# Kernel optimization log

Measured on AMD Instinct MI355X. Metric: run time of the kernel, lower is better.

The kernel has to match this reference:

```python
import jax, jax.numpy as jnp
import numpy as np

B, K, T, H, D = 16, 49, 256, 512, 512


def setup_inputs() -> dict:
    key = jax.random.key(0)
    ks = jax.random.split(key, 8)
    s = 1.0 / np.sqrt(H)
    return {
        "V": jax.random.normal(ks[0], (B, K, H), jnp.float32),
        "h_t": jax.random.normal(ks[1], (B, T, H), jnp.float32),
        "s_t": jax.random.normal(ks[2], (B, T, H), jnp.float32),
        "Wv": jax.random.normal(ks[3], (H, D), jnp.float32) * s,
        "bv": jnp.zeros((D,), jnp.float32),
        "Wg": jax.random.normal(ks[4], (H, D), jnp.float32) * s,
        "bg": jnp.zeros((D,), jnp.float32),
        "Ws": jax.random.normal(ks[5], (H, D), jnp.float32) * s,
        "bs": jnp.zeros((D,), jnp.float32),
        "Wh": jax.random.normal(ks[6], (D, 1), jnp.float32) * (1.0 / np.sqrt(D)),
        "bh": jnp.zeros((1,), jnp.float32),
    }


def reference(V, h_t, s_t, Wv, bv, Wg, bg, Ws, bs, Wh, bh):
    # projections (dropout is identity in eval)
    cv = V @ Wv + bv                        # [B, K, D]
    cg = h_t @ Wg + bg                      # [B, T, D]
    # content_v: [B, T, K, D] via broadcast add
    content_v = cv[:, None, :, :] + cg[:, :, None, :]
    z_t = (jnp.tanh(content_v) @ Wh + bh)[..., 0]   # [B, T, K]
    alpha_t = jax.nn.softmax(z_t, axis=-1)          # [B, T, K]
    c_t = jnp.einsum('btk,bkh->bth', alpha_t, V)    # [B, T, H]
    # sentinel branch
    content_s = (s_t @ Ws + bs) + cg                # [B, T, D]
    z_ext = jnp.tanh(content_s) @ Wh + bh           # [B, T, 1]
    extended = jnp.concatenate([z_t, z_ext], axis=-1)  # [B, T, K+1]
    alpha_hat = jax.nn.softmax(extended, axis=-1)
    beta_t = alpha_hat[:, :, -1:]                   # [B, T, 1]
    c_hat_t = beta_t * s_t + (1.0 - beta_t) * c_t   # [B, T, H]
    return (c_hat_t, alpha_t, beta_t)
```

## Files before the change

kernel.cpp:

```cpp
#include <hip/hip_runtime.h>
#include <hip/hip_fp16.h>
#include <cstdint>
#include <cstddef>

#define B_ 16
#define K_ 49
#define T_ 256
#define H_ 512
#define D_ 512

#define TANH_SCALE 2.8853900817779268f
#define LOG2E 1.4426950408889634f

typedef _Float16 half8 __attribute__((ext_vector_type(8)));
typedef float floatx4 __attribute__((ext_vector_type(4)));

#define ROWS_A 9088
#define OFF_V 0
#define OFF_H 896
#define OFF_S 4992

__device__ __forceinline__ void async16(const _Float16* g, const _Float16* l) {
    __builtin_amdgcn_global_load_lds(
        (const __attribute__((address_space(1))) unsigned int*)g,
        (__attribute__((address_space(3))) unsigned int*)l, 16, 0, 0);
}

__global__ __launch_bounds__(256) void conv_all(const float* __restrict__ V,
                                                const float* __restrict__ h_t,
                                                const float* __restrict__ s_t,
                                                const float* __restrict__ Wv,
                                                const float* __restrict__ Wg,
                                                const float* __restrict__ Ws,
                                                _Float16* __restrict__ Af16,
                                                _Float16* __restrict__ Wt) {
    __shared__ float tile[32][33];
    int tid = threadIdx.x;
    if (blockIdx.x < 2272) {
        int idx = (blockIdx.x * 256 + tid) * 8;
        int row = idx >> 9;
        int col = idx & 511;
        const float* src;
        if (row < 784)        src = V   + (size_t)row * 512 + col;
        else if (row < 896)   src = nullptr;
        else if (row < 4992)  src = h_t + (size_t)(row - 896) * 512 + col;
        else                  src = s_t + (size_t)(row - 4992) * 512 + col;
        half8 h;
        if (src) {
            float4 f0 = *(const float4*)(src);
            float4 f1 = *(const float4*)(src + 4);
            h[0] = (_Float16)f0.x; h[1] = (_Float16)f0.y;
            h[2] = (_Float16)f0.z; h[3] = (_Float16)f0.w;
            h[4] = (_Float16)f1.x; h[5] = (_Float16)f1.y;
            h[6] = (_Float16)f1.z; h[7] = (_Float16)f1.w;
        } else {
            h = (half8)((_Float16)0.0f);
        }
        *(half8*)(Af16 + idx) = h;
    } else {
        int bid = blockIdx.x - 2272;
        int p = bid >> 8;
        int rem = bid & 255;
        int bx = rem & 15, by = rem >> 4;
        const float* W = (p == 0) ? Wv : (p == 1) ? Wg : Ws;
        _Float16* outp = Wt + (size_t)p * 512 * 512;
        int tx = tid & 31, ty = tid >> 5;
        int c = bx * 32 + tx;
        int rbase = by * 32;
#pragma unroll
        for (int i = 0; i < 4; i++)
            tile[ty + i * 8][tx] = W[(size_t)(rbase + ty + i * 8) * 512 + c];
        __syncthreads();
        int k = rbase + tx;
#pragma unroll
        for (int i = 0; i < 4; i++) {
            int n = bx * 32 + ty + i * 8;
            outp[(size_t)n * 512 + k] = (_Float16)(tile[tx][ty + i * 8] * TANH_SCALE);
        }
    }
}

__global__ __launch_bounds__(256) void gemm_f16(
    const _Float16* __restrict__ Af16, const _Float16* __restrict__ Wt,
    const float* __restrict__ bv, const float* __restrict__ bg2,
    const float* __restrict__ bs, float* __restrict__ cv,
    float* __restrict__ cg, float* __restrict__ cs) {
    __shared__ __align__(16) _Float16 As[2][64 * 64];
    __shared__ __align__(16) _Float16 Bs[2][64 * 64];

    int bid = blockIdx.x;
    int id = (bid & 7) * 142 + (bid >> 3);

    int rowbase; const _Float16* Bt; const float* bias; float* C;
    if (id < 112)       { rowbase = OFF_V;            Bt = Wt;          bias = bv;  C = cv; }
    else if (id < 624)  { id -= 112; rowbase = OFF_H; Bt = Wt + 262144; bias = bg2; C = cg; }
    else                { id -= 624; rowbase = OFF_S; Bt = Wt + 524288; bias = bs;  C = cs; }
    int tm = id >> 3, tn = id & 7;

    int tid = threadIdx.x;
    int wave = tid >> 6, lane = tid & 63;

    const _Float16* gA[2]; int ldsOff[2];
    const _Float16* gB[2];
#pragma unroll
    for (int i = 0; i < 2; i++) {
        int p = i * 256 + tid;
        int ks = p >> 8, x = (p >> 6) & 3, q = (p >> 4) & 3, f = p & 15;
        gA[i] = Af16 + (size_t)(rowbase + tm * 64 + x * 16 + f) * 512 + ks * 32 + q * 8;
        gB[i] = Bt   + (size_t)(tn * 64 + x * 16 + f) * 512 + ks * 32 + q * 8;
        ldsOff[i] = p * 8;
    }

    floatx4 acc[4];
#pragma unroll
    for (int x = 0; x < 4; x++) acc[x] = (floatx4)0.0f;

#pragma unroll
    for (int i = 0; i < 2; i++) async16(gA[i], &As[0][ldsOff[i]]);
#pragma unroll
    for (int i = 0; i < 2; i++) async16(gB[i], &Bs[0][ldsOff[i]]);
    __syncthreads();

    for (int kk = 0; kk < 8; kk++) {
        int cur = kk & 1;
        if (kk < 7) {
#pragma unroll
            for (int i = 0; i < 2; i++) async16(gA[i] + (kk + 1) * 64, &As[cur ^ 1][ldsOff[i]]);
#pragma unroll
            for (int i = 0; i < 2; i++) async16(gB[i] + (kk + 1) * 64, &Bs[cur ^ 1][ldsOff[i]]);
        }

#pragma unroll
        for (int ks = 0; ks < 2; ks++) {
            half8 a[4];
#pragma unroll
            for (int x = 0; x < 4; x++)
                a[x] = *(const half8*)&As[cur][(ks * 256 + x * 64 + lane) * 8];
            half8 b = *(const half8*)&Bs[cur][(ks * 256 + wave * 64 + lane) * 8];
#pragma unroll
            for (int x = 0; x < 4; x++)
                acc[x] = __builtin_amdgcn_mfma_f32_16x16x32_f16(a[x], b, acc[x], 0, 0, 0);
        }

        if (kk < 7) __syncthreads();
    }

    int dn = lane & 15, dq = lane >> 4;
    int colg = tn * 64 + wave * 16 + dn;
    float bc = bias[colg] * TANH_SCALE;
#pragma unroll
    for (int x = 0; x < 4; x++) {
        int rowg = tm * 64 + x * 16 + dq * 4;
#pragma unroll
        for (int r = 0; r < 4; r++)
            C[(size_t)(rowg + r) * 512 + colg] = __builtin_amdgcn_exp2f(acc[x][r] + bc);
    }
}

__device__ __forceinline__ float wave_sum(float v) {
#pragma unroll
    for (int o = 32; o > 0; o >>= 1) v += __shfl_xor(v, o);
    return v;
}
__device__ __forceinline__ float wave_max(float v) {
#pragma unroll
    for (int o = 32; o > 0; o >>= 1) v = fmaxf(v, __shfl_xor(v, o));
    return v;
}

__device__ __forceinline__ float xsum4(float a0, float a1, float a2, float a3, int lane) {
    bool hi = (lane & 32) != 0;
    float t0 = hi ? a0 : a2;
    float t1 = hi ? a1 : a3;
    t0 = __shfl_xor(t0, 32);
    t1 = __shfl_xor(t1, 32);
    if (hi) { a0 = t0; a1 = t1; } else { a2 = t0; a3 = t1; }
    bool h2 = (lane & 16) != 0;
    float u0 = h2 ? a0 : a1;
    float u1 = h2 ? a2 : a3;
    u0 = __shfl_xor(u0, 16);
    u1 = __shfl_xor(u1, 16);
    if (h2) { a0 = u0; a2 = u1; } else { a1 = u0; a3 = u1; }
    float s = (a0 + a1) + (a2 + a3);
#pragma unroll
    for (int o = 8; o > 0; o >>= 1) s += __shfl_xor(s, o);
    return s;
}

#define TB 4
__global__ __launch_bounds__(256) void z_kernel(
    const float* __restrict__ ecv, const float* __restrict__ ecg,
    const float* __restrict__ ecs, const float* __restrict__ V,
    const float* __restrict__ s_t, const float* __restrict__ Wh,
    const float* __restrict__ bh, float* __restrict__ out) {
    int bx = blockIdx.x;
    int b  = bx >> 6;
    int t0 = (bx & 63) << 2;
    int bt0 = b * 256 + t0;
    int tid = threadIdx.x;
    int wave = tid >> 6, lane = tid & 63;

    __shared__ float zl[TB][64];
    __shared__ float4 al4[52];
    __shared__ float bl[TB];

    float whv[8], egv[TB][8];
#pragma unroll
    for (int j = 0; j < 8; j++) whv[j] = Wh[j * 64 + lane];
#pragma unroll
    for (int tt = 0; tt < TB; tt++) {
        const float* cgp = ecg + (size_t)(bt0 + tt) * 512;
#pragma unroll
        for (int j = 0; j < 8; j++) egv[tt][j] = cgp[j * 64 + lane];
    }
    float s8 = 0.0f;
#pragma unroll
    for (int j = 0; j < 8; j++) s8 += whv[j];
    float zbase = wave_sum(s8) + bh[0];

    float rv[8], rn[8];
    {
        const float* rp = ecv + (size_t)(b * 49 + wave) * 512;
#pragma unroll
        for (int j = 0; j < 8; j++) rv[j] = rp[j * 64 + lane];
    }
    for (int task = wave; task < 49; task += 4) {
        int nt = task + 4;
        if (nt < 49) {
            const float* rp = ecv + (size_t)(b * 49 + nt) * 512;
#pragma unroll
            for (int j = 0; j < 8; j++) rn[j] = rp[j * 64 + lane];
        }
        float acc[TB] = {0.0f, 0.0f, 0.0f, 0.0f};
#pragma unroll
        for (int tt = 0; tt < TB; tt++) {
#pragma unroll
            for (int j = 0; j < 8; j++) {
                float t = fmaf(rv[j], egv[tt][j], 1.0f);
                float r = __builtin_amdgcn_rcpf(t);
                acc[tt] = fmaf(whv[j], r, acc[tt]);
            }
        }
        float z = xsum4(acc[0], acc[1], acc[2], acc[3], lane);
        if ((lane & 15) == 0) zl[lane >> 4][task] = zbase - 2.0f * z;
#pragma unroll
        for (int j = 0; j < 8; j++) rv[j] = rn[j];
    }
#pragma unroll
    for (int tt = 0; tt < TB; tt++) {
        if (wave == tt) {
            const float* rp = ecs + (size_t)(bt0 + tt) * 512;
            float acc = 0.0f;
#pragma unroll
            for (int j = 0; j < 8; j++) {
                float t = fmaf(rp[j * 64 + lane], egv[tt][j], 1.0f);
                float r = __builtin_amdgcn_rcpf(t);
                acc = fmaf(whv[j], r, acc);
            }
            float s = wave_sum(acc);
            if (lane == 0) zl[tt][49] = zbase - 2.0f * s;
        }
    }
    __syncthreads();

    {
        int w = wave;
        float z = (lane < 49) ? zl[w][lane] : -3.0e38f;
        float m = wave_max(z);
        float e = (lane < 49) ? __builtin_amdgcn_exp2f((z - m) * LOG2E) : 0.0f;
        float s = wave_sum(e);
        float zext = zl[w][49];
        float m2 = fmaxf(m, zext);
        float sc   = __builtin_amdgcn_exp2f((m - m2) * LOG2E);
        float eext = __builtin_amdgcn_exp2f((zext - m2) * LOG2E);
        float s2 = s * sc + eext;
        float beta = eext / s2;
        if (lane < 49) {
            float a = e / s;
            ((float*)&al4[lane])[w] = a;
            out[(size_t)B_ * T_ * H_ + (size_t)(bt0 + w) * 49 + lane] = a;
        }
        if (lane == 0) {
            bl[w] = beta;
            out[(size_t)B_ * T_ * H_ + (size_t)B_ * T_ * K_ + (bt0 + w)] = beta;
        }
    }
    __syncthreads();

    const float* Vb = V + (size_t)b * 49 * 512;
    float2 accA[TB];
#pragma unroll
    for (int tt = 0; tt < TB; tt++) accA[tt] = make_float2(0.0f, 0.0f);
#pragma unroll 7
    for (int k = 0; k < 49; k++) {
        float4 a4 = al4[k];
        float2 v = *(const float2*)(Vb + (size_t)k * 512 + tid * 2);
        accA[0].x = fmaf(a4.x, v.x, accA[0].x);  accA[0].y = fmaf(a4.x, v.y, accA[0].y);
        accA[1].x = fmaf(a4.y, v.x, accA[1].x);  accA[1].y = fmaf(a4.y, v.y, accA[1].y);
        accA[2].x = fmaf(a4.z, v.x, accA[2].x);  accA[2].y = fmaf(a4.z, v.y, accA[2].y);
        accA[3].x = fmaf(a4.w, v.x, accA[3].x);  accA[3].y = fmaf(a4.w, v.y, accA[3].y);
    }
#pragma unroll
    for (int tt = 0; tt < TB; tt++) {
        float beta = bl[tt];
        float2 sp = *(const float2*)(s_t + (size_t)(bt0 + tt) * 512 + tid * 2);
        float2 o;
        o.x = beta * sp.x + (1.0f - beta) * accA[tt].x;
        o.y = beta * sp.y + (1.0f - beta) * accA[tt].y;
        *(float2*)(out + (size_t)(bt0 + tt) * 512 + tid * 2) = o;
    }
}

extern "C" void kernel_launch(void* const* d_in, const int* in_sizes, int n_in,
                              void* d_out, int out_size, void* d_ws, size_t ws_size,
                              hipStream_t stream) {
    const float* V   = (const float*)d_in[0];
    const float* h_t = (const float*)d_in[1];
    const float* s_t = (const float*)d_in[2];
    const float* Wv  = (const float*)d_in[3];
    const float* bv  = (const float*)d_in[4];
    const float* Wg  = (const float*)d_in[5];
    const float* bg  = (const float*)d_in[6];
    const float* Ws  = (const float*)d_in[7];
    const float* bs  = (const float*)d_in[8];
    const float* Wh  = (const float*)d_in[9];
    const float* bh  = (const float*)d_in[10];
    float* out = (float*)d_out;

    char* ws = (char*)d_ws;
    _Float16* Af16 = (_Float16*)(ws);
    _Float16* Wt   = (_Float16*)(ws + 9306112);
    float* ecv = (float*)(ws + 10878976);
    float* ecg = (float*)(ws + 12713984);
    float* ecs = (float*)(ws + 21102592);

    conv_all<<<3040, 256, 0, stream>>>(V, h_t, s_t, Wv, Wg, Ws, Af16, Wt);
    gemm_f16<<<1136, 256, 0, stream>>>(Af16, Wt, bv, bg, bs, ecv, ecg, ecs);
    z_kernel<<<1024, 256, 0, stream>>>(ecv, ecg, ecs, V, s_t, Wh, bh, out);
}
```

Baseline: 135.7 us.

## Pre-tile fp16 operands into MFMA fragment layout and single-barrier pipeline

The conversion kernel now writes activations and transposed weights in a blocked layout that matches the LDS fragment order, so each GEMM tile stage becomes one contiguous 8KB chunk read with fully coalesced async loads. The GEMM main loop is restructured to use a single explicit vmcnt wait plus barrier per stage, with sched_barriers, and is fully unrolled. This removes strided global reads and one barrier per iteration. The cost is a more complex index computation in the pre-pass, which now does scattered fp16 weight stores.

```diff
diff --git a/kernel.cpp b/kernel.cpp
--- a/kernel.cpp
+++ b/kernel.cpp
@@ -56,14 +56,16 @@
         } else {
             h = (half8)((_Float16)0.0f);
         }
-        *(half8*)(Af16 + idx) = h;
+        int t  = row >> 7, x8 = (row >> 4) & 7, f = row & 15;
+        int kk = col >> 5, q  = (col >> 3) & 3;
+        size_t off = (size_t)t * 65536 + (size_t)kk * 4096 + (size_t)(x8 * 64 + q * 16 + f) * 8;
+        *(half8*)(Af16 + off) = h;
     } else {
         int bid = blockIdx.x - 2272;
         int p = bid >> 8;
         int rem = bid & 255;
         int bx = rem & 15, by = rem >> 4;
         const float* W = (p == 0) ? Wv : (p == 1) ? Wg : Ws;
-        _Float16* outp = Wt + (size_t)p * 512 * 512;
         int tx = tid & 31, ty = tid >> 5;
         int c = bx * 32 + tx;
         int rbase = by * 32;
@@ -72,10 +74,14 @@
             tile[ty + i * 8][tx] = W[(size_t)(rbase + ty + i * 8) * 512 + c];
         __syncthreads();
         int k = rbase + tx;
+        int kk = k >> 5, q = (k >> 3) & 3, e = k & 7;
 #pragma unroll
         for (int i = 0; i < 4; i++) {
             int n = bx * 32 + ty + i * 8;
-            outp[(size_t)n * 512 + k] = (_Float16)(tile[tx][ty + i * 8] * TANH_SCALE);
+            int nt = n >> 7, x8 = (n >> 4) & 7, f = n & 15;
+            size_t off = (size_t)p * 262144 + (size_t)nt * 65536 + (size_t)kk * 4096
+                       + (size_t)(x8 * 64 + q * 16 + f) * 8 + e;
+            Wt[off] = (_Float16)(tile[tx][ty + i * 8] * TANH_SCALE);
         }
     }
 }
@@ -85,8 +91,8 @@
     const float* __restrict__ bv, const float* __restrict__ bg2,
     const float* __restrict__ bs, float* __restrict__ cv,
     float* __restrict__ cg, float* __restrict__ cs) {
-    __shared__ __align__(16) _Float16 As[2][64 * 64];
-    __shared__ __align__(16) _Float16 Bs[2][64 * 64];
+    __shared__ __align__(16) _Float16 As[2][4096];
+    __shared__ __align__(16) _Float16 Bs[2][4096];
 
     int bid = blockIdx.x;
     int id = (bid & 7) * 142 + (bid >> 3);
@@ -100,15 +106,16 @@
     int tid = threadIdx.x;
     int wave = tid >> 6, lane = tid & 63;
 
-    const _Float16* gA[2]; int ldsOff[2];
-    const _Float16* gB[2];
+    int r0 = rowbase + tm * 64;
+    const _Float16* aBase = Af16 + (size_t)(r0 >> 7) * 65536 + (size_t)((r0 >> 6) & 1) * 2048;
+    const _Float16* bBase = Bt   + (size_t)(tn >> 1) * 65536 + (size_t)(tn & 1) * 2048;
+
+    const _Float16* gA[2]; const _Float16* gB[2]; int ldsOff[2];
 #pragma unroll
     for (int i = 0; i < 2; i++) {
-        int p = i * 256 + tid;
-        int ks = p >> 8, x = (p >> 6) & 3, q = (p >> 4) & 3, f = p & 15;
-        gA[i] = Af16 + (size_t)(rowbase + tm * 64 + x * 16 + f) * 512 + ks * 32 + q * 8;
-        gB[i] = Bt   + (size_t)(tn * 64 + x * 16 + f) * 512 + ks * 32 + q * 8;
-        ldsOff[i] = p * 8;
+        gA[i] = aBase + (size_t)i * 4096 + (size_t)tid * 8;
+        gB[i] = bBase + (size_t)i * 4096 + (size_t)tid * 8;
+        ldsOff[i] = (i * 256 + tid) * 8;
     }
 
     floatx4 acc[4];
@@ -119,16 +126,21 @@
     for (int i = 0; i < 2; i++) async16(gA[i], &As[0][ldsOff[i]]);
 #pragma unroll
     for (int i = 0; i < 2; i++) async16(gB[i], &Bs[0][ldsOff[i]]);
-    __syncthreads();
-
-    for (int kk = 0; kk < 8; kk++) {
-        int cur = kk & 1;
-        if (kk < 7) {
-#pragma unroll
-            for (int i = 0; i < 2; i++) async16(gA[i] + (kk + 1) * 64, &As[cur ^ 1][ldsOff[i]]);
-#pragma unroll
-            for (int i = 0; i < 2; i++) async16(gB[i] + (kk + 1) * 64, &Bs[cur ^ 1][ldsOff[i]]);
-        }
+
+#pragma unroll
+    for (int s = 0; s < 8; s++) {
+        const int cur = s & 1;
+        asm volatile("s_waitcnt vmcnt(0)" ::: "memory");
+        __builtin_amdgcn_s_barrier();
+        __builtin_amdgcn_sched_barrier(0);
+
+        if (s < 7) {
+#pragma unroll
+            for (int i = 0; i < 2; i++) async16(gA[i] + (s + 1) * 8192, &As[cur ^ 1][ldsOff[i]]);
+#pragma unroll
+            for (int i = 0; i < 2; i++) async16(gB[i] + (s + 1) * 8192, &Bs[cur ^ 1][ldsOff[i]]);
+        }
+        __builtin_amdgcn_sched_barrier(0);
 
 #pragma unroll
         for (int ks = 0; ks < 2; ks++) {
@@ -141,8 +153,6 @@
             for (int x = 0; x < 4; x++)
                 acc[x] = __builtin_amdgcn_mfma_f32_16x16x32_f16(a[x], b, acc[x], 0, 0, 0);
         }
-
-        if (kk < 7) __syncthreads();
     }
 
     int dn = lane & 15, dq = lane >> 4;
```

After: 127.6 us. -5.9%, faster.
